# Kernel tuning notes

Measured on AMD Instinct MI355X. Metric: run time of the kernel, lower is better.

The kernel has to match this reference:

```python
import jax, jax.numpy as jnp
import numpy as np

SCALE = 16.0  # init kwarg: scale
B, S, D = 8, 2048, 256  # Q == S (self-attention style ragged masking)


def setup_inputs() -> dict:
    key = jax.random.key(0)
    k1, k2, k3 = jax.random.split(key, 3)
    context = jax.random.normal(k1, (B, S, D), dtype=jnp.float32)
    query = jax.random.normal(k2, (B, S, D), dtype=jnp.float32)
    # lengths in [1, S] so no row is fully masked (avoids NaN softmax)
    length = jax.random.randint(k3, (B,), 1, S + 1, dtype=jnp.int64)
    return {"context": context, "query": query, "length": length}


def reference(context, query, length):
    # raw_scores: [B, Q, S]
    raw = jnp.einsum("bqd,bsd->bqs", query, context) / SCALE
    pos = jnp.arange(raw.shape[2])  # [S]
    key_valid = pos[None, :] < length[:, None]            # [B, S]
    raw = jnp.where(key_valid[:, None, :], raw, -jnp.inf)  # mask key positions
    scores = jax.nn.softmax(raw, axis=2)
    row_valid = (jnp.arange(raw.shape[1])[None, :] < length[:, None])  # [B, Q]
    scores = scores * row_valid[:, :, None].astype(scores.dtype)       # zero padded query rows
    attended = jnp.einsum("bqs,bsd->bqd", scores, context)  # values defaults to context
    return attended, scores
```

## Files before the change

### kernel.cpp

```cpp
#include <hip/hip_runtime.h>
#include <hip/hip_bf16.h>

#define NB 8
#define SS 2048
#define DD 256
#define SCALE_INV 0.0625f

typedef __attribute__((ext_vector_type(8))) short bf16x8;
typedef __attribute__((ext_vector_type(4))) float f32x4;

#define MFMA __builtin_amdgcn_mfma_f32_16x16x32_bf16

static __device__ __forceinline__ unsigned short f2bf(float f) {
  unsigned int u = __builtin_bit_cast(unsigned int, f);
  u += 0x7FFFu + ((u >> 16) & 1u);
  return (unsigned short)(u >> 16);
}
static __device__ __forceinline__ float bf2f(unsigned short s) {
  unsigned int u = ((unsigned int)s) << 16;
  return __builtin_bit_cast(float, u);
}

static __device__ __forceinline__ void gll16(const void* g, void* l) {
  __builtin_amdgcn_global_load_lds(
      (const __attribute__((address_space(1))) unsigned int*)g,
      (__attribute__((address_space(3))) unsigned int*)l, 16, 0, 0);
}

static __device__ __forceinline__ int load_len(const int* lp, int b) {
  bool is64 = ((lp[1] | lp[3] | lp[5] | lp[7]) == 0);
  return is64 ? lp[2 * b] : lp[b];
}

__global__ __launch_bounds__(256)
void preconv(const float* __restrict__ ctx,
             unsigned short* __restrict__ cbf,
             unsigned short* __restrict__ cT)
{
  __shared__ unsigned short T[64][68];
  const int tid = threadIdx.x;
  const int s0 = blockIdx.x * 64, d0 = blockIdx.y * 64, b = blockIdx.z;
  const int r = tid >> 4, c4 = tid & 15;

  #pragma unroll
  for (int i = 0; i < 4; ++i) {
    int row = i * 16 + r;
    size_t gi = ((size_t)(b * SS + s0 + row)) * DD + d0 + c4 * 4;
    float4 v = *(const float4*)(ctx + gi);
    ushort4 o;
    o.x = f2bf(v.x); o.y = f2bf(v.y); o.z = f2bf(v.z); o.w = f2bf(v.w);
    *(ushort4*)(cbf + gi) = o;
    T[c4 * 4 + 0][row] = o.x;
    T[c4 * 4 + 1][row] = o.y;
    T[c4 * 4 + 2][row] = o.z;
    T[c4 * 4 + 3][row] = o.w;
  }
  __syncthreads();
  const int rr = tid >> 2, cc = tid & 3;
  #pragma unroll
  for (int j = 0; j < 4; ++j) {
    size_t go = ((size_t)(b * DD + d0 + rr)) * SS + s0 + cc * 16 + j * 4;
    *(ushort4*)(cT + go) = *(const ushort4*)&T[rr][cc * 16 + j * 4];
  }
}

#define LB0   0
#define LB1   32768
#define LPP0  65536
#define LPP1  70144
#define LINV  74752
#define LSMEM 74880

__global__ __launch_bounds__(256, 2)
void attn_v11(const unsigned short* __restrict__ cbf,
              const unsigned short* __restrict__ cT,
              const float* __restrict__ qry,
              const int* __restrict__ lenp,
              float* __restrict__ att,
              float* __restrict__ sc)
{
  __shared__ __align__(16) unsigned char smem[LSMEM];

  const int tid = threadIdx.x;
  const int wv = tid >> 6;
  const int lane = tid & 63;
  const int l15 = lane & 15;
  const int l4 = lane >> 4;
  const int sl = wv * 16 + l15;

  int lens_[8];
  #pragma unroll
  for (int i = 0; i < 8; ++i) lens_[i] = load_len(lenp, i);
  int ord[8] = {0, 1, 2, 3, 4, 5, 6, 7};
  for (int i = 1; i < 8; ++i) {
    int key = ord[i], kl = lens_[key], j = i - 1;
    while (j >= 0 && lens_[ord[j]] < kl) { ord[j + 1] = ord[j]; --j; }
    ord[j + 1] = key;
  }
  const int wg = blockIdx.x;
  const int r0 = (wg < 256) ? wg : 767 - wg;
  const int b = ord[r0 >> 6];
  const int q0 = (r0 & 63) * 32;
  const int bq = b * SS + q0;
  const int len = lens_[b];

  if (q0 >= len) {
    float4 z = {0.f, 0.f, 0.f, 0.f};
    for (int row = 0; row < 32; ++row) {
      float4* sp = (float4*)(sc + (size_t)(bq + row) * SS);
      for (int c = tid; c < 512; c += 256) sp[c] = z;
    }
    float4* ap = (float4*)(att + (size_t)bq * DD);
    for (int c = tid; c < 2048; c += 256) ap[c] = z;
    return;
  }

  const int nt_act = (len + 63) >> 6;
  const char* cbf_b = (const char*)cbf + (size_t)b * SS * DD * 2;
  const char* cT_b  = (const char*)cT  + (size_t)b * SS * DD * 2;
  char* scr = (char*)sc + (size_t)bq * SS * 4 + 4096;

  auto stage_cs = [&](unsigned char* buf, int st) {
    const char* gb = cbf_b + ((size_t)st << 15);
    #pragma unroll
    for (int rr = 0; rr < 8; ++rr) {
      int chunk = rr * 256 + tid;
      int s = chunk >> 5, c = chunk & 31;
      gll16(gb + ((size_t)s << 9) + ((c ^ (s & 7)) << 4), buf + chunk * 16);
    }
  };
  auto stage_ct = [&](unsigned char* buf, int st) {
    const char* gb = cT_b + st * 128;
    #pragma unroll
    for (int rr = 0; rr < 8; ++rr) {
      int chunk = rr * 256 + tid;
      int d = chunk >> 3, c = chunk & 7;
      gll16(gb + (size_t)d * 4096 + ((c ^ (d & 7)) << 4), buf + chunk * 16);
    }
  };
  auto stage_p = [&](unsigned char* buf, int st) {
    const char* gb = scr + (size_t)st * 128;
    gll16(gb + (size_t)(tid >> 3) * 8192 + ((tid & 7) << 4), buf + tid * 16);
  };

  bf16x8 qf[2][8];
  {
    const float* qb = qry + ((size_t)b * SS + q0) * DD;
    #pragma unroll
    for (int qi = 0; qi < 2; ++qi)
      #pragma unroll
      for (int kk = 0; kk < 8; ++kk) {
        const float4* qp = (const float4*)(qb + (size_t)(qi * 16 + l15) * DD + kk * 32 + l4 * 8);
        float4 x = qp[0], y = qp[1];
        bf16x8 f;
        f[0] = (short)f2bf(x.x); f[1] = (short)f2bf(x.y);
        f[2] = (short)f2bf(x.z); f[3] = (short)f2bf(x.w);
        f[4] = (short)f2bf(y.x); f[5] = (short)f2bf(y.y);
        f[6] = (short)f2bf(y.z); f[7] = (short)f2bf(y.w);
        qf[qi][kk] = f;
      }
  }

  float ps0[4] = {0.f, 0.f, 0.f, 0.f};
  float ps1[4] = {0.f, 0.f, 0.f, 0.f};
  unsigned short* Ps = (unsigned short*)(smem + LPP0);

  stage_cs(smem + LB0, 0);

  for (int t = 0; t < nt_act; ++t) {
    __syncthreads();
    unsigned char* cur = (t & 1) ? (smem + LB1) : (smem + LB0);
    if (t + 1 < nt_act) stage_cs((t & 1) ? (smem + LB0) : (smem + LB1), t + 1);

    f32x4 a0 = {0.f, 0.f, 0.f, 0.f}, a1 = {0.f, 0.f, 0.f, 0.f};
    const unsigned char* rowp = cur + sl * 512;
    #pragma unroll
    for (int kk = 0; kk < 8; ++kk) {
      bf16x8 bfr = *(const bf16x8*)(rowp + (((kk * 4 + l4) ^ (sl & 7)) << 4));
      a0 = MFMA(qf[0][kk], bfr, a0, 0, 0, 0);
      a1 = MFMA(qf[1][kk], bfr, a1, 0, 0, 0);
    }
    bool sval = (t * 64 + sl) < len;
    #pragma unroll
    for (int qi = 0; qi < 2; ++qi) {
      #pragma unroll
      for (int j = 0; j < 4; ++j) {
        int row = qi * 16 + l4 * 4 + j;
        float e = sval ? __expf((qi ? a1[j] : a0[j]) * SCALE_INV) : 0.f;
        if (qi == 0) ps0[j] += e; else ps1[j] += e;
        Ps[row * 72 + sl] = f2bf(e);
      }
    }
    __syncthreads();

    {
      int rr = tid >> 3, sb = tid & 7;
      bf16x8 v = *(const bf16x8*)(Ps + rr * 72 + sb * 8);
      *(bf16x8*)(scr + (size_t)rr * 8192 + (size_t)t * 128 + ((sb ^ (rr & 7)) << 4)) = v;
    }
  }

  #pragma unroll
  for (int off = 1; off < 16; off <<= 1)
    #pragma unroll
    for (int j = 0; j < 4; ++j) {
      ps0[j] += __shfl_xor(ps0[j], off, 64);
      ps1[j] += __shfl_xor(ps1[j], off, 64);
    }
  float* part = (float*)(smem + LPP1);
  if (l15 == 0) {
    #pragma unroll
    for (int j = 0; j < 4; ++j) {
      part[wv * 32 + l4 * 4 + j] = ps0[j];
      part[wv * 32 + 16 + l4 * 4 + j] = ps1[j];
    }
  }
  __syncthreads();
  float* invs = (float*)(smem + LINV);
  if (tid < 32) {
    float rs = part[tid] + part[32 + tid] + part[64 + tid] + part[96 + tid];
    invs[tid] = (q0 + tid < len) ? (1.0f / fmaxf(rs, 1e-30f)) : 0.f;
  }

  f32x4 av0[4] = {{0.f,0.f,0.f,0.f},{0.f,0.f,0.f,0.f},{0.f,0.f,0.f,0.f},{0.f,0.f,0.f,0.f}};
  f32x4 av1[4] = {{0.f,0.f,0.f,0.f},{0.f,0.f,0.f,0.f},{0.f,0.f,0.f,0.f},{0.f,0.f,0.f,0.f}};

  stage_p(smem + LPP0, 0);
  stage_ct(smem + LB0, 0);

  for (int t = 0; t < nt_act; ++t) {
    __syncthreads();
    unsigned char* curP = (t & 1) ? (smem + LPP1) : (smem + LPP0);
    unsigned char* curC = (t & 1) ? (smem + LB1) : (smem + LB0);
    if (t + 1 < nt_act) {
      stage_p((t & 1) ? (smem + LPP0) : (smem + LPP1), t + 1);
      stage_ct((t & 1) ? (smem + LB0) : (smem + LB1), t + 1);
    }

    bf16x8 pa0[2], pa1[2], cb[4][2];
    #pragma unroll
    for (int k2 = 0; k2 < 2; ++k2) {
      pa0[k2] = *(const bf16x8*)(curP + l15 * 128 + (((k2 * 4 + l4) ^ (l15 & 7)) << 4));
      pa1[k2] = *(const bf16x8*)(curP + (16 + l15) * 128 + (((k2 * 4 + l4) ^ (l15 & 7)) << 4));
      #pragma unroll
      for (int nt = 0; nt < 4; ++nt) {
        int d = wv * 64 + nt * 16 + l15;
        cb[nt][k2] = *(const bf16x8*)(curC + d * 128 + (((k2 * 4 + l4) ^ (d & 7)) << 4));
      }
    }

    {
      int rr = tid >> 3, cbk = tid & 7;
      int sb = cbk ^ (rr & 7);
      bf16x8 pv = *(const bf16x8*)(curP + rr * 128 + cbk * 16);
      float inv0 = invs[rr];
      float4 f0, f1;
      f0.x = bf2f((unsigned short)pv[0]) * inv0; f0.y = bf2f((unsigned short)pv[1]) * inv0;
      f0.z = bf2f((unsigned short)pv[2]) * inv0; f0.w = bf2f((unsigned short)pv[3]) * inv0;
      f1.x = bf2f((unsigned short)pv[4]) * inv0; f1.y = bf2f((unsigned short)pv[5]) * inv0;
      f1.z = bf2f((unsigned short)pv[6]) * inv0; f1.w = bf2f((unsigned short)pv[7]) * inv0;
      float* sp = sc + (size_t)(bq + rr) * SS + t * 64 + sb * 8;
      *(float4*)sp = f0;
      *(float4*)(sp + 4) = f1;
    }

    #pragma unroll
    for (int k2 = 0; k2 < 2; ++k2)
      #pragma unroll
      for (int nt = 0; nt < 4; ++nt) {
        av0[nt] = MFMA(pa0[k2], cb[nt][k2], av0[nt], 0, 0, 0);
        av1[nt] = MFMA(pa1[k2], cb[nt][k2], av1[nt], 0, 0, 0);
      }
  }

  {
    int s_start = nt_act * 64;
    int rem4 = (SS - s_start) >> 2;
    if (rem4 > 0) {
      __syncthreads();
      float4 z = {0.f, 0.f, 0.f, 0.f};
      for (int row = 0; row < 32; ++row)
        for (int c = tid; c < rem4; c += 256)
          *(float4*)(sc + (size_t)(bq + row) * SS + s_start + c * 4) = z;
    }
  }

  #pragma unroll
  for (int nt = 0; nt < 4; ++nt)
    #pragma unroll
    for (int j = 0; j < 4; ++j) {
      int col = wv * 64 + nt * 16 + l15;
      int row0 = l4 * 4 + j;
      att[(size_t)(bq + row0) * DD + col] = av0[nt][j] * invs[row0];
      att[(size_t)(bq + 16 + row0) * DD + col] = av1[nt][j] * invs[16 + row0];
    }
}

extern "C" void kernel_launch(void* const* d_in, const int* in_sizes, int n_in,
                              void* d_out, int out_size, void* d_ws, size_t ws_size,
                              hipStream_t stream) {
  const float* ctx = (const float*)d_in[0];
  const float* qry = (const float*)d_in[1];
  const int* len = (const int*)d_in[2];
  float* att = (float*)d_out;
  float* sc = att + (size_t)NB * SS * DD;

  const size_t nqd = (size_t)NB * SS * DD;
  const size_t need = nqd * 4;

  if (ws_size >= need) {
    unsigned short* cbf = (unsigned short*)d_ws;
    unsigned short* cTp = cbf + nqd;
    preconv<<<dim3(SS / 64, DD / 64, NB), dim3(256), 0, stream>>>(ctx, cbf, cTp);
    attn_v11<<<dim3(512), dim3(256), 0, stream>>>(cbf, cTp, qry, len, att, sc);
  }
}
```

Measured before the change: 71.86 us.

## Process 64 query rows per 512-thread block sharing staged context tiles

Doubles the query tile per workgroup to 64 rows by using 8 waves split into two 32-row halves. Both halves share each staged context and transposed-context tile, which halves the global and LDS staging traffic per query row. The grid shrinks to 256 blocks with a simple batch-interleaved mapping, and the per-block length sorting and reversed scheduling used for load balancing are removed. This risks worse tail imbalance across ragged lengths, and the larger dynamic LDS footprint may limit occupancy.

```diff
diff --git a/kernel.cpp b/kernel.cpp
--- a/kernel.cpp
+++ b/kernel.cpp
@@ -10,6 +10,14 @@
 typedef __attribute__((ext_vector_type(4))) float f32x4;
 
 #define MFMA __builtin_amdgcn_mfma_f32_16x16x32_bf16
+
+#define OB0   0
+#define OB1   32768
+#define OPPA  65536
+#define OPPB  73728
+#define OPART 81920
+#define OINV  82944
+#define SMEMB 83200
 
 static __device__ __forceinline__ unsigned short f2bf(float f) {
   unsigned int u = __builtin_bit_cast(unsigned int, f);
@@ -64,54 +72,37 @@
   }
 }
 
-#define LB0   0
-#define LB1   32768
-#define LPP0  65536
-#define LPP1  70144
-#define LINV  74752
-#define LSMEM 74880
-
-__global__ __launch_bounds__(256, 2)
-void attn_v11(const unsigned short* __restrict__ cbf,
+__global__ __launch_bounds__(512, 2)
+void attn_v12(const unsigned short* __restrict__ cbf,
               const unsigned short* __restrict__ cT,
               const float* __restrict__ qry,
               const int* __restrict__ lenp,
               float* __restrict__ att,
               float* __restrict__ sc)
 {
-  __shared__ __align__(16) unsigned char smem[LSMEM];
+  extern __shared__ __align__(16) unsigned char smem[];
 
   const int tid = threadIdx.x;
   const int wv = tid >> 6;
+  const int qh = wv >> 2;
+  const int wvk = wv & 3;
   const int lane = tid & 63;
   const int l15 = lane & 15;
   const int l4 = lane >> 4;
-  const int sl = wv * 16 + l15;
-
-  int lens_[8];
-  #pragma unroll
-  for (int i = 0; i < 8; ++i) lens_[i] = load_len(lenp, i);
-  int ord[8] = {0, 1, 2, 3, 4, 5, 6, 7};
-  for (int i = 1; i < 8; ++i) {
-    int key = ord[i], kl = lens_[key], j = i - 1;
-    while (j >= 0 && lens_[ord[j]] < kl) { ord[j + 1] = ord[j]; --j; }
-    ord[j + 1] = key;
-  }
+  const int sl = wvk * 16 + l15;
+
   const int wg = blockIdx.x;
-  const int r0 = (wg < 256) ? wg : 767 - wg;
-  const int b = ord[r0 >> 6];
-  const int q0 = (r0 & 63) * 32;
+  const int b = wg & 7;
+  const int q0 = (wg >> 3) * 64;
   const int bq = b * SS + q0;
-  const int len = lens_[b];
+  const int len = load_len(lenp, b);
 
   if (q0 >= len) {
     float4 z = {0.f, 0.f, 0.f, 0.f};
-    for (int row = 0; row < 32; ++row) {
-      float4* sp = (float4*)(sc + (size_t)(bq + row) * SS);
-      for (int c = tid; c < 512; c += 256) sp[c] = z;
-    }
+    for (int row = 0; row < 64; ++row)
+      *((float4*)(sc + (size_t)(bq + row) * SS) + tid) = z;
     float4* ap = (float4*)(att + (size_t)bq * DD);
-    for (int c = tid; c < 2048; c += 256) ap[c] = z;
+    for (int c = tid; c < 4096; c += 512) ap[c] = z;
     return;
   }
 
@@ -123,8 +114,8 @@
   auto stage_cs = [&](unsigned char* buf, int st) {
     const char* gb = cbf_b + ((size_t)st << 15);
     #pragma unroll
-    for (int rr = 0; rr < 8; ++rr) {
-      int chunk = rr * 256 + tid;
+    for (int rr = 0; rr < 4; ++rr) {
+      int chunk = rr * 512 + tid;
       int s = chunk >> 5, c = chunk & 31;
       gll16(gb + ((size_t)s << 9) + ((c ^ (s & 7)) << 4), buf + chunk * 16);
     }
@@ -132,8 +123,8 @@
   auto stage_ct = [&](unsigned char* buf, int st) {
     const char* gb = cT_b + st * 128;
     #pragma unroll
-    for (int rr = 0; rr < 8; ++rr) {
-      int chunk = rr * 256 + tid;
+    for (int rr = 0; rr < 4; ++rr) {
+      int chunk = rr * 512 + tid;
       int d = chunk >> 3, c = chunk & 7;
       gll16(gb + (size_t)d * 4096 + ((c ^ (d & 7)) << 4), buf + chunk * 16);
     }
@@ -145,7 +136,7 @@
 
   bf16x8 qf[2][8];
   {
-    const float* qb = qry + ((size_t)b * SS + q0) * DD;
+    const float* qb = qry + ((size_t)(bq + qh * 32)) * DD;
     #pragma unroll
     for (int qi = 0; qi < 2; ++qi)
       #pragma unroll
@@ -163,14 +154,16 @@
 
   float ps0[4] = {0.f, 0.f, 0.f, 0.f};
   float ps1[4] = {0.f, 0.f, 0.f, 0.f};
-  unsigned short* Ps = (unsigned short*)(smem + LPP0);
-
-  stage_cs(smem + LB0, 0);
+  unsigned short* PsA = (unsigned short*)(smem + OPPA);
+  unsigned short* PsB = (unsigned short*)(smem + OPPB);
+  unsigned short* Psh = qh ? PsB : PsA;
+
+  stage_cs(smem + OB0, 0);
 
   for (int t = 0; t < nt_act; ++t) {
     __syncthreads();
-    unsigned char* cur = (t & 1) ? (smem + LB1) : (smem + LB0);
-    if (t + 1 < nt_act) stage_cs((t & 1) ? (smem + LB0) : (smem + LB1), t + 1);
+    unsigned char* cur = (t & 1) ? (smem + OB1) : (smem + OB0);
+    if (t + 1 < nt_act) stage_cs((t & 1) ? (smem + OB0) : (smem + OB1), t + 1);
 
     f32x4 a0 = {0.f, 0.f, 0.f, 0.f}, a1 = {0.f, 0.f, 0.f, 0.f};
     const unsigned char* rowp = cur + sl * 512;
@@ -185,17 +178,18 @@
     for (int qi = 0; qi < 2; ++qi) {
       #pragma unroll
       for (int j = 0; j < 4; ++j) {
-        int row = qi * 16 + l4 * 4 + j;
+        int row32 = qi * 16 + l4 * 4 + j;
         float e = sval ? __expf((qi ? a1[j] : a0[j]) * SCALE_INV) : 0.f;
         if (qi == 0) ps0[j] += e; else ps1[j] += e;
-        Ps[row * 72 + sl] = f2bf(e);
+        Psh[row32 * 72 + sl] = f2bf(e);
       }
     }
     __syncthreads();
 
     {
       int rr = tid >> 3, sb = tid & 7;
-      bf16x8 v = *(const bf16x8*)(Ps + rr * 72 + sb * 8);
+      const unsigned short* Psrc = ((rr >> 5) ? PsB : PsA) + (rr & 31) * 72 + sb * 8;
+      bf16x8 v = *(const bf16x8*)Psrc;
       *(bf16x8*)(scr + (size_t)rr * 8192 + (size_t)t * 128 + ((sb ^ (rr & 7)) << 4)) = v;
     }
   }
@@ -207,44 +201,45 @@
       ps0[j] += __shfl_xor(ps0[j], off, 64);
       ps1[j] += __shfl_xor(ps1[j], off, 64);
     }
-  float* part = (float*)(smem + LPP1);
+  float* part = (float*)(smem + OPART);
   if (l15 == 0) {
     #pragma unroll
     for (int j = 0; j < 4; ++j) {
-      part[wv * 32 + l4 * 4 + j] = ps0[j];
-      part[wv * 32 + 16 + l4 * 4 + j] = ps1[j];
+      part[qh * 128 + wvk * 32 + l4 * 4 + j] = ps0[j];
+      part[qh * 128 + wvk * 32 + 16 + l4 * 4 + j] = ps1[j];
     }
   }
   __syncthreads();
-  float* invs = (float*)(smem + LINV);
-  if (tid < 32) {
-    float rs = part[tid] + part[32 + tid] + part[64 + tid] + part[96 + tid];
+  float* invs = (float*)(smem + OINV);
+  if (tid < 64) {
+    const float* ph = part + (tid >> 5) * 128;
+    int r32 = tid & 31;
+    float rs = ph[r32] + ph[32 + r32] + ph[64 + r32] + ph[96 + r32];
     invs[tid] = (q0 + tid < len) ? (1.0f / fmaxf(rs, 1e-30f)) : 0.f;
   }
+  stage_p(smem + OPPA, 0);
+  stage_ct(smem + OB0, 0);
 
   f32x4 av0[4] = {{0.f,0.f,0.f,0.f},{0.f,0.f,0.f,0.f},{0.f,0.f,0.f,0.f},{0.f,0.f,0.f,0.f}};
   f32x4 av1[4] = {{0.f,0.f,0.f,0.f},{0.f,0.f,0.f,0.f},{0.f,0.f,0.f,0.f},{0.f,0.f,0.f,0.f}};
 
-  stage_p(smem + LPP0, 0);
-  stage_ct(smem + LB0, 0);
-
   for (int t = 0; t < nt_act; ++t) {
     __syncthreads();
-    unsigned char* curP = (t & 1) ? (smem + LPP1) : (smem + LPP0);
-    unsigned char* curC = (t & 1) ? (smem + LB1) : (smem + LB0);
+    unsigned char* curP = (t & 1) ? (smem + OPPB) : (smem + OPPA);
+    unsigned char* curC = (t & 1) ? (smem + OB1) : (smem + OB0);
     if (t + 1 < nt_act) {
-      stage_p((t & 1) ? (smem + LPP0) : (smem + LPP1), t + 1);
-      stage_ct((t & 1) ? (smem + LB0) : (smem + LB1), t + 1);
+      stage_p((t & 1) ? (smem + OPPA) : (smem + OPPB), t + 1);
+      stage_ct((t & 1) ? (smem + OB0) : (smem + OB1), t + 1);
     }
 
     bf16x8 pa0[2], pa1[2], cb[4][2];
     #pragma unroll
     for (int k2 = 0; k2 < 2; ++k2) {
-      pa0[k2] = *(const bf16x8*)(curP + l15 * 128 + (((k2 * 4 + l4) ^ (l15 & 7)) << 4));
-      pa1[k2] = *(const bf16x8*)(curP + (16 + l15) * 128 + (((k2 * 4 + l4) ^ (l15 & 7)) << 4));
+      pa0[k2] = *(const bf16x8*)(curP + (qh * 32 + l15) * 128 + (((k2 * 4 + l4) ^ (l15 & 7)) << 4));
+      pa1[k2] = *(const bf16x8*)(curP + (qh * 32 + 16 + l15) * 128 + (((k2 * 4 + l4) ^ (l15 & 7)) << 4));
       #pragma unroll
       for (int nt = 0; nt < 4; ++nt) {
-        int d = wv * 64 + nt * 16 + l15;
+        int d = wvk * 64 + nt * 16 + l15;
         cb[nt][k2] = *(const bf16x8*)(curC + d * 128 + (((k2 * 4 + l4) ^ (d & 7)) << 4));
       }
     }
@@ -279,8 +274,8 @@
     if (rem4 > 0) {
       __syncthreads();
       float4 z = {0.f, 0.f, 0.f, 0.f};
-      for (int row = 0; row < 32; ++row)
-        for (int c = tid; c < rem4; c += 256)
+      for (int row = 0; row < 64; ++row)
+        for (int c = tid; c < rem4; c += 512)
           *(float4*)(sc + (size_t)(bq + row) * SS + s_start + c * 4) = z;
     }
   }
@@ -289,8 +284,8 @@
   for (int nt = 0; nt < 4; ++nt)
     #pragma unroll
     for (int j = 0; j < 4; ++j) {
-      int col = wv * 64 + nt * 16 + l15;
-      int row0 = l4 * 4 + j;
+      int col = wvk * 64 + nt * 16 + l15;
+      int row0 = qh * 32 + l4 * 4 + j;
       att[(size_t)(bq + row0) * DD + col] = av0[nt][j] * invs[row0];
       att[(size_t)(bq + 16 + row0) * DD + col] = av1[nt][j] * invs[16 + row0];
     }
@@ -312,6 +307,6 @@
     unsigned short* cbf = (unsigned short*)d_ws;
     unsigned short* cTp = cbf + nqd;
     preconv<<<dim3(SS / 64, DD / 64, NB), dim3(256), 0, stream>>>(ctx, cbf, cTp);
-    attn_v11<<<dim3(512), dim3(256), 0, stream>>>(cbf, cTp, qry, len, att, sc);
-  }
-}
+    attn_v12<<<dim3(NB * 32), dim3(512), SMEMB, stream>>>(cbf, cTp, qry, len, att, sc);
+  }
+}
```

Result: slower. 77.86 us (+8.3%).
